# Performance work log

Measured on AMD Instinct MI355X. Metric: run time of the kernel, lower is better.

The kernel has to match this reference:

```python
import jax, jax.numpy as jnp
import numpy as np

B, L, H = 4, 1024, 8192
NH, HD = 64, 128
PD = HD // 2  # 64, rope-style positional dim
QL = HD * 4 * 3  # 1536, Q latent dim
KVL = HD * 4     # 512, KV latent dim


def setup_inputs() -> dict:
    key = jax.random.key(0)
    ks = jax.random.split(key, 18)
    w = lambda k, i, o: (jax.random.normal(k, (i, o), jnp.float32) * (1.0 / np.sqrt(i))).astype(jnp.float32)
    b = lambda k, o: jnp.zeros((o,), jnp.float32)
    return {
        'x': jax.random.normal(ks[0], (B, L, H), jnp.float32),
        'W_dq': w(ks[1], H, QL),   'b_dq': b(ks[2], QL),
        'W_dkv': w(ks[3], H, KVL), 'b_dkv': b(ks[4], KVL),
        'W_uq': w(ks[5], QL, H),   'b_uq': b(ks[6], H),
        'W_uk': w(ks[7], KVL, H),  'b_uk': b(ks[8], H),
        'W_uv': w(ks[9], KVL, H),  'b_uv': b(ks[10], H),
        'W_pq': w(ks[11], QL, NH * PD), 'b_pq': b(ks[12], NH * PD),
        'W_pk': w(ks[13], H, PD),  'b_pk': b(ks[14], PD),
        'W_o': w(ks[15], H, H),    'b_o': b(ks[16], H),
    }


def reference(x, W_dq, b_dq, W_dkv, b_dkv, W_uq, b_uq, W_uk, b_uk,
              W_uv, b_uv, W_pq, b_pq, W_pk, b_pk, W_o, b_o):
    Bb, Ll, Hh = x.shape
    # low-rank latents
    Q_lat = x @ W_dq + b_dq          # (B, L, 1536)
    KV_lat = x @ W_dkv + b_dkv       # (B, L, 512)
    # up-projections
    Q_c = (Q_lat @ W_uq + b_uq).reshape(Bb, Ll, NH, HD)
    Q_r = (Q_lat @ W_pq + b_pq).reshape(Bb, Ll, NH, PD)
    Q = jnp.concatenate([Q_c, Q_r], axis=-1)            # (B, L, NH, 192)
    K_c = (KV_lat @ W_uk + b_uk).reshape(Bb, Ll, NH, HD)
    K_r = x @ W_pk + b_pk                                # (B, L, 64), shared across heads
    K_r = jnp.broadcast_to(K_r[:, :, None, :], (Bb, Ll, NH, PD))
    K = jnp.concatenate([K_c, K_r], axis=-1)             # (B, L, NH, 192)
    V = (KV_lat @ W_uv + b_uv).reshape(Bb, Ll, NH, HD)   # (B, L, NH, 128)
    # attention with mismatched Q/K (192) vs V (128) head dims; scale by sqrt(128)
    scores = jnp.einsum('bqhd,bkhd->bhqk', Q, K) / np.float32(np.sqrt(HD))
    causal = jnp.tril(jnp.ones((Ll, Ll), bool))
    scores = jnp.where(causal, scores, jnp.float32(-jnp.inf))
    attn = jax.nn.softmax(scores, axis=-1)               # dropout = identity (eval)
    out = jnp.einsum('bhqk,bkhd->bqhd', attn, V).reshape(Bb, Ll, Hh)
    return out @ W_o + b_o
```

## Files before the change

### kernel.cpp

```cpp
#include <hip/hip_runtime.h>
#include <cstdint>

typedef unsigned short u16;
typedef __attribute__((ext_vector_type(8))) short bf16x8;
typedef __attribute__((ext_vector_type(4))) float f32x4;
typedef __attribute__((ext_vector_type(4))) unsigned short u16x4;

__device__ __forceinline__ u16 f2b(float f) {
  union { float f; uint32_t u; } v; v.f = f;
  uint32_t r = v.u + 0x7FFFu + ((v.u >> 16) & 1u);
  return (u16)(r >> 16);
}

__device__ __forceinline__ void gload_lds16(const void* g, void* l) {
  __builtin_amdgcn_global_load_lds((const __attribute__((address_space(1))) void*)g,
                                   (__attribute__((address_space(3))) void*)l, 16, 0, 0);
}

__device__ __forceinline__ void barrier_raw() {
  __builtin_amdgcn_sched_barrier(0);
  asm volatile("" ::: "memory");
  __builtin_amdgcn_s_barrier();
  asm volatile("" ::: "memory");
  __builtin_amdgcn_sched_barrier(0);
}
__device__ __forceinline__ void wait_vm8() {
  asm volatile("s_waitcnt vmcnt(8)" ::: "memory");
  __builtin_amdgcn_sched_barrier(0);
}

__global__ __launch_bounds__(256) void cvt_bf16(const float* __restrict__ in,
                                                u16* __restrict__ out, long n) {
  long i = ((long)blockIdx.x * 256 + threadIdx.x) * 4;
  if (i >= n) return;
  f32x4 v = *(const f32x4*)(in + i);
  u16x4 o;
#pragma unroll
  for (int k = 0; k < 4; k++) o[k] = f2b(v[k]);
  *(u16x4*)(out + i) = o;
}

__global__ __launch_bounds__(256) void transpose_cvt(const float* __restrict__ W,
                                                     u16* __restrict__ WT, int K, int N) {
  __shared__ float tile[32][33];
  const int tn0 = blockIdx.x * 32;
  const int tk0 = blockIdx.y * 32;
  const int c = threadIdx.x & 31;
  const int r0 = threadIdx.x >> 5;
#pragma unroll
  for (int rr = 0; rr < 32; rr += 8)
    tile[r0 + rr][c] = W[(long)(tk0 + r0 + rr) * N + tn0 + c];
  __syncthreads();
#pragma unroll
  for (int rr = 0; rr < 32; rr += 8)
    WT[(long)(tn0 + r0 + rr) * K + tk0 + c] = f2b(tile[c][r0 + rr]);
}

__global__ __launch_bounds__(256) void biascat3(const float* __restrict__ a,
                                                const float* __restrict__ b,
                                                const float* __restrict__ c,
                                                float* __restrict__ o) {
  int i = blockIdx.x * 256 + threadIdx.x;
  if (i < 1536) o[i] = a[i];
  else if (i < 2048) o[i] = b[i - 1536];
  else if (i < 2112) o[i] = c[i - 2048];
}
__global__ __launch_bounds__(256) void biascat2(const float* __restrict__ a,
                                                const float* __restrict__ b,
                                                int na, int n, float* __restrict__ o) {
  int i = blockIdx.x * 256 + threadIdx.x;
  if (i >= n) return;
  o[i] = (i < na) ? a[i] : b[i - na];
}

__global__ __launch_bounds__(256) void latcombine(const float* __restrict__ p,
                                                  const float* __restrict__ bias,
                                                  u16* __restrict__ lat) {
  const long S = 4096L * 2112;
  long i = ((long)blockIdx.x * 256 + threadIdx.x) * 4;
  if (i >= S) return;
  f32x4 s0 = *(const f32x4*)(p + i);
  f32x4 s1 = *(const f32x4*)(p + S + i);
  f32x4 s2 = *(const f32x4*)(p + 2 * S + i);
  f32x4 s3 = *(const f32x4*)(p + 3 * S + i);
  const int n = (int)(i % 2112);
  u16x4 o;
#pragma unroll
  for (int k = 0; k < 4; k++) o[k] = f2b(s0[k] + s1[k] + s2[k] + s3[k] + bias[n + k]);
  *(u16x4*)(lat + i) = o;
}

__global__ __launch_bounds__(256) void repl_kr(const u16* __restrict__ Kr,
                                               u16* __restrict__ Kbuf, int stride) {
  long idx = (long)blockIdx.x * 256 + threadIdx.x;
  int d4 = idx & 15;
  long t = idx >> 4;
  int hh = t & 63;
  long tok = t >> 6;
  if (tok >= 4096) return;
  u16x4 v = *(const u16x4*)(Kr + tok * (long)stride + d4 * 4);
  long b = tok >> 10, l = tok & 1023;
  *(u16x4*)(Kbuf + ((b * 64 + hh) * 1024 + l) * 192 + 128 + d4 * 4) = v;
}

template<int MODE>
__global__ __launch_bounds__(512, 2) void gemm256(
    const u16* __restrict__ A, long lda, const u16* __restrict__ BT, long ldb,
    const float* __restrict__ bias, void* __restrict__ outp, void* __restrict__ outp2,
    int N, int K) {
  __shared__ u16 sA[2][2][8192];
  __shared__ u16 sB[2][2][8192];
  const int tid = threadIdx.x;
  const int lane = tid & 63;
  const int w = tid >> 6;
  const int wr = w >> 2, wc = w & 3;
  const int hi = lane >> 4, lo = lane & 15;

  const int Nt = gridDim.x, Mt = gridDim.y;
  const int bid = blockIdx.y * Nt + blockIdx.x;
  const int xcd = bid & 7;
  const int idx = bid >> 3;
  int mt, nt;
  if ((Nt & 1) == 0) {
    const int Rm = Mt >> 2, Rn = Nt >> 1;
    const int xr = xcd & 3, xcn = xcd >> 2;
    const int Wb = Rn < 8 ? Rn : 8;
    const int cb = idx / (Rm * Wb);
    const int rem = idx - cb * (Rm * Wb);
    mt = xr * Rm + (rem % Rm);
    nt = xcn * Rn + cb * Wb + rem / Rm;
  } else {
    const int Rm = Mt >> 3;
    const int Wb = Nt < 8 ? Nt : 8;
    const int cb = idx / (Rm * Wb);
    const int rem = idx - cb * (Rm * Wb);
    mt = xcd * Rm + (rem % Rm);
    nt = cb * Wb + rem / Rm;
  }
  const long m0 = (long)mt * 256;
  const long n0 = (long)nt * 256;

  const int nkt = K >> 6;
  const long kb = (long)blockIdx.z * K;

  const int srow = tid >> 2;
  const int scol = ((tid & 3) ^ ((tid >> 3) & 3)) * 8;
  const long arow0 = m0 + srow, arow1 = arow0 + 128;
  long brow0 = n0 + srow, brow1 = brow0 + 128;
  if (brow0 > N - 1) brow0 = N - 1;
  if (brow1 > N - 1) brow1 = N - 1;
  const u16* aS0 = A + arow0 * lda + kb + scol;
  const u16* aS1 = A + arow1 * lda + kb + scol;
  const u16* bS0 = BT + brow0 * ldb + kb + scol;
  const u16* bS1 = BT + brow1 * ldb + kb + scol;

  const int aRd = (wr * 128 + lo) * 32 + (hi ^ ((lo >> 1) & 3)) * 8;
  const int bRd = (wc * 64 + lo) * 32 + (hi ^ ((lo >> 1) & 3)) * 8;

  f32x4 acc[8][4] = {};

#define STAGE(s0, s1, koff, dst) do { \
    gload_lds16((s0) + (koff), (dst) + tid * 8); \
    gload_lds16((s1) + (koff), (dst) + 4096 + tid * 8); \
  } while (0)
#define LDA_F(bufr, kh, m) (*(const bf16x8*)(&sA[bufr][kh][aRd + (m) * 512]))
#define LDB_F(bufr, kh, n) (*(const bf16x8*)(&sB[bufr][kh][bRd + (n) * 512]))
#define MFMA_GRP(mi, av) \
    acc[mi][0] = __builtin_amdgcn_mfma_f32_16x16x32_bf16(av, b0, acc[mi][0], 0, 0, 0); \
    acc[mi][1] = __builtin_amdgcn_mfma_f32_16x16x32_bf16(av, b1, acc[mi][1], 0, 0, 0); \
    acc[mi][2] = __builtin_amdgcn_mfma_f32_16x16x32_bf16(av, b2, acc[mi][2], 0, 0, 0); \
    acc[mi][3] = __builtin_amdgcn_mfma_f32_16x16x32_bf16(av, b3, acc[mi][3], 0, 0, 0);

  STAGE(aS0, aS1, 0, &sA[0][0][0]);
  STAGE(bS0, bS1, 0, &sB[0][0][0]);
  STAGE(aS0, aS1, 32, &sA[0][1][0]);
  STAGE(bS0, bS1, 32, &sB[0][1][0]);
  {
    const long t1o = (nkt > 1) ? 64 : 0;
    STAGE(aS0, aS1, t1o, &sA[1][0][0]);
    STAGE(bS0, bS1, t1o, &sB[1][0][0]);
  }
  wait_vm8();
  barrier_raw();

  for (int t = 0; t < nkt; ++t) {
    const int cur = t & 1, nxt = cur ^ 1;
    const int t1c = (t + 1 < nkt) ? t + 1 : nkt - 1;
    const int t2c = (t + 2 < nkt) ? t + 2 : nkt - 1;
    const long o1 = (long)t1c * 64;
    const long o2 = (long)t2c * 64;
    bf16x8 b0, b1, b2, b3, a0, a1, a2, a3, a4, a5, a6, a7;
    b0 = LDB_F(cur, 0, 0); b1 = LDB_F(cur, 0, 1); b2 = LDB_F(cur, 0, 2); b3 = LDB_F(cur, 0, 3);
    a0 = LDA_F(cur, 0, 0); a1 = LDA_F(cur, 0, 1); a2 = LDA_F(cur, 0, 2); a3 = LDA_F(cur, 0, 3);
    a4 = LDA_F(cur, 0, 4); a5 = LDA_F(cur, 0, 5); a6 = LDA_F(cur, 0, 6); a7 = LDA_F(cur, 0, 7);
    STAGE(aS0, aS1, o1 + 32, &sA[nxt][1][0]);
    barrier_raw();
    __builtin_amdgcn_s_setprio(1);
    MFMA_GRP(0, a0) MFMA_GRP(1, a1) MFMA_GRP(2, a2) MFMA_GRP(3, a3)
    __builtin_amdgcn_s_setprio(0);
    STAGE(bS0, bS1, o1 + 32, &sB[nxt][1][0]);
    __builtin_amdgcn_s_setprio(1);
    MFMA_GRP(4, a4) MFMA_GRP(5, a5) MFMA_GRP(6, a6) MFMA_GRP(7, a7)
    __builtin_amdgcn_s_setprio(0);
    wait_vm8();
    barrier_raw();
    b0 = LDB_F(cur, 1, 0); b1 = LDB_F(cur, 1, 1); b2 = LDB_F(cur, 1, 2); b3 = LDB_F(cur, 1, 3);
    a0 = LDA_F(cur, 1, 0); a1 = LDA_F(cur, 1, 1); a2 = LDA_F(cur, 1, 2); a3 = LDA_F(cur, 1, 3);
    a4 = LDA_F(cur, 1, 4); a5 = LDA_F(cur, 1, 5); a6 = LDA_F(cur, 1, 6); a7 = LDA_F(cur, 1, 7);
    STAGE(aS0, aS1, o2, &sA[cur][0][0]);
    barrier_raw();
    __builtin_amdgcn_s_setprio(1);
    MFMA_GRP(0, a0) MFMA_GRP(1, a1) MFMA_GRP(2, a2) MFMA_GRP(3, a3)
    __builtin_amdgcn_s_setprio(0);
    STAGE(bS0, bS1, o2, &sB[cur][0][0]);
    __builtin_amdgcn_s_setprio(1);
    MFMA_GRP(4, a4) MFMA_GRP(5, a5) MFMA_GRP(6, a6) MFMA_GRP(7, a7)
    __builtin_amdgcn_s_setprio(0);
    wait_vm8();
    barrier_raw();
  }
  asm volatile("s_waitcnt vmcnt(0)" ::: "memory");

#undef STAGE
#undef LDA_F
#undef LDB_F
#undef MFMA_GRP

#pragma unroll
  for (int m = 0; m < 8; m++) {
#pragma unroll
    for (int n = 0; n < 4; n++) {
      const long mb = m0 + wr * 128 + m * 16 + hi * 4;
      const long nn = n0 + wc * 64 + n * 16 + lo;
      if (nn >= N) continue;
      const float bv = bias[nn];
      if (MODE == 0) {
#pragma unroll
        for (int r = 0; r < 4; r++)
          ((u16*)outp)[(mb + r) * (long)N + nn] = f2b(acc[m][n][r] + bv);
      } else if (MODE == 3) {
#pragma unroll
        for (int r = 0; r < 4; r++)
          ((float*)outp)[(mb + r) * (long)N + nn] = acc[m][n][r] + bv;
      } else if (MODE == 6) {
        float* po = (float*)outp + (size_t)blockIdx.z * (4096ULL * 2112ULL);
#pragma unroll
        for (int r = 0; r < 4; r++)
          po[(mb + r) * (long)N + nn] = acc[m][n][r];
      } else if (MODE == 4) {
        if (nn < 8192) {
          const long h = nn >> 7, d = nn & 127;
#pragma unroll
          for (int r = 0; r < 4; r++) {
            const long mm = mb + r;
            const long bq = mm >> 10, l = mm & 1023;
            ((u16*)outp)[((bq * 64 + h) * 1024 + l) * 192 + d] = f2b(acc[m][n][r] + bv);
          }
        } else {
          const long q = nn - 8192;
          const long h = q >> 6, d = q & 63;
#pragma unroll
          for (int r = 0; r < 4; r++) {
            const long mm = mb + r;
            const long bq = mm >> 10, l = mm & 1023;
            ((u16*)outp)[((bq * 64 + h) * 1024 + l) * 192 + 128 + d] = f2b(acc[m][n][r] + bv);
          }
        }
      } else {
        if (nn < 8192) {
          const long h = nn >> 7, d = nn & 127;
#pragma unroll
          for (int r = 0; r < 4; r++) {
            const long mm = mb + r;
            const long bq = mm >> 10, l = mm & 1023;
            ((u16*)outp)[((bq * 64 + h) * 1024 + l) * 192 + d] = f2b(acc[m][n][r] + bv);
          }
        } else {
          const long v = nn - 8192;
          const long h = v >> 7, d = v & 127;
          u16x4 pk;
#pragma unroll
          for (int r = 0; r < 4; r++) pk[r] = f2b(acc[m][n][r] + bv);
          const long bq = mb >> 10, l = mb & 1023;
          *(u16x4*)((u16*)outp2 + ((bq * 64 + h) * 128 + d) * 1024 + l) = pk;
        }
      }
    }
  }
}

__global__ __launch_bounds__(512, 2) void attn256(const u16* __restrict__ Qb,
                                                  const u16* __restrict__ Kb,
                                                  const u16* __restrict__ Vt,
                                                  u16* __restrict__ O) {
  __shared__ u16 sK[2][12288];
  __shared__ u16 sV[2][8192];
  __shared__ u16 P[8][32][72];
  const int bh = blockIdx.x;
  const int qtb = 3 - blockIdx.y;
  const int b = bh >> 6, h = bh & 63;
  const int tid = threadIdx.x, w = tid >> 6, lane = tid & 63;
  const int hi = lane >> 4, lo = lane & 15, lo7 = lane & 7;
  const int q0w = qtb * 256 + w * 32;
  const u16* Qh = Qb + (size_t)bh * 1024 * 192;
  const u16* Kh = Kb + (size_t)bh * 1024 * 192;
  const u16* Vh = Vt + (size_t)bh * 128 * 1024;
  const float scale = 0.08838834764831845f;
  const float NEGINF = -3.0e38f;

  int kOff0, kOff1, kOff2, vOff0, vOff1;
  {
    int g0 = tid, g1 = tid + 512, g2 = tid + 1024;
    int r0 = g0 / 24, r1 = g1 / 24, r2 = g2 / 24;
    kOff0 = r0 * 192 + ((g0 - r0 * 24) ^ (r0 & 7)) * 8;
    kOff1 = r1 * 192 + ((g1 - r1 * 24) ^ (r1 & 7)) * 8;
    kOff2 = r2 * 192 + ((g2 - r2 * 24) ^ (r2 & 7)) * 8;
    int s0 = tid, s1 = tid + 512;
    vOff0 = (s0 >> 3) * 1024 + ((s0 & 7) ^ ((s0 >> 3) & 7)) * 8;
    vOff1 = (s1 >> 3) * 1024 + ((s1 & 7) ^ ((s1 >> 3) & 7)) * 8;
  }
#define STAGE_KV(tt, bb) do { \
    const u16* kb_ = Kh + (size_t)(tt) * (64 * 192); \
    const u16* vb_ = Vh + (size_t)(tt) * 64; \
    gload_lds16(kb_ + kOff0, &sK[bb][0] + tid * 8); \
    gload_lds16(kb_ + kOff1, &sK[bb][4096] + tid * 8); \
    gload_lds16(kb_ + kOff2, &sK[bb][8192] + tid * 8); \
    gload_lds16(vb_ + vOff0, &sV[bb][0] + tid * 8); \
    gload_lds16(vb_ + vOff1, &sV[bb][4096] + tid * 8); \
  } while (0)

  bf16x8 qf[2][6];
#pragma unroll
  for (int qi = 0; qi < 2; qi++) {
    const u16* qp = Qh + (size_t)(q0w + qi * 16 + lo) * 192 + hi * 8;
#pragma unroll
    for (int f = 0; f < 6; f++) qf[qi][f] = *(const bf16x8*)(qp + f * 32);
  }

  f32x4 oacc[2][8] = {};
  float m_run[2][4], l_run[2][4];
#pragma unroll
  for (int qi = 0; qi < 2; qi++)
#pragma unroll
    for (int r = 0; r < 4; r++) { m_run[qi][r] = NEGINF; l_run[qi][r] = 0.f; }

  const int nkt = (qtb + 1) * 4;
  STAGE_KV(0, 0);
  __syncthreads();

  for (int t = 0; t < nkt; t++) {
    const int cur = t & 1;
    const int tn = (t + 1 < nkt) ? t + 1 : nkt - 1;
    STAGE_KV(tn, cur ^ 1);
    const int k0 = t * 64;
    if (k0 < q0w + 32) {
      f32x4 s[2][4] = {};
      __builtin_amdgcn_s_setprio(1);
#pragma unroll
      for (int j = 0; j < 4; j++) {
#pragma unroll
        for (int f = 0; f < 6; f++) {
          bf16x8 kf = *(const bf16x8*)(&sK[cur][((j * 16 + lo) * 24 + ((f * 4 + hi) ^ lo7)) * 8]);
          s[0][j] = __builtin_amdgcn_mfma_f32_16x16x32_bf16(qf[0][f], kf, s[0][j], 0, 0, 0);
          s[1][j] = __builtin_amdgcn_mfma_f32_16x16x32_bf16(qf[1][f], kf, s[1][j], 0, 0, 0);
        }
      }
      __builtin_amdgcn_s_setprio(0);
      const bool diag = (k0 + 63 > q0w);
#pragma unroll
      for (int qi = 0; qi < 2; qi++) {
#pragma unroll
        for (int r = 0; r < 4; r++) {
          const int q = q0w + qi * 16 + hi * 4 + r;
          float sv[4];
          float mx = NEGINF;
#pragma unroll
          for (int j = 0; j < 4; j++) {
            float v = s[qi][j][r] * scale;
            if (diag && (k0 + j * 16 + lo > q)) v = NEGINF;
            sv[j] = v;
            mx = fmaxf(mx, v);
          }
#pragma unroll
          for (int o = 1; o < 16; o <<= 1) mx = fmaxf(mx, __shfl_xor(mx, o, 64));
          const float mnew = fmaxf(m_run[qi][r], mx);
          float sum = 0.f;
#pragma unroll
          for (int j = 0; j < 4; j++) {
            float pv = __expf(sv[j] - mnew);
            sum += pv;
            P[w][qi * 16 + hi * 4 + r][j * 16 + lo] = f2b(pv);
          }
#pragma unroll
          for (int o = 1; o < 16; o <<= 1) sum += __shfl_xor(sum, o, 64);
          const float alpha = __expf(m_run[qi][r] - mnew);
          l_run[qi][r] = l_run[qi][r] * alpha + sum;
          m_run[qi][r] = mnew;
#pragma unroll
          for (int j = 0; j < 8; j++) oacc[qi][j][r] *= alpha;
        }
      }
      __builtin_amdgcn_s_setprio(1);
#pragma unroll
      for (int kk = 0; kk < 2; kk++) {
        bf16x8 pf0 = *(const bf16x8*)(&P[w][lo][kk * 32 + hi * 8]);
        bf16x8 pf1 = *(const bf16x8*)(&P[w][16 + lo][kk * 32 + hi * 8]);
#pragma unroll
        for (int j = 0; j < 8; j++) {
          bf16x8 vf = *(const bf16x8*)(&sV[cur][((j * 16 + lo) * 8 + ((kk * 4 + hi) ^ lo7)) * 8]);
          oacc[0][j] = __builtin_amdgcn_mfma_f32_16x16x32_bf16(pf0, vf, oacc[0][j], 0, 0, 0);
          oacc[1][j] = __builtin_amdgcn_mfma_f32_16x16x32_bf16(pf1, vf, oacc[1][j], 0, 0, 0);
        }
      }
      __builtin_amdgcn_s_setprio(0);
    }
    __syncthreads();
  }
#undef STAGE_KV

#pragma unroll
  for (int qi = 0; qi < 2; qi++) {
#pragma unroll
    for (int r = 0; r < 4; r++) {
      const float inv = 1.f / l_run[qi][r];
      const int q = q0w + qi * 16 + hi * 4 + r;
      u16* op = O + ((size_t)(b * 1024 + q) * 64 + h) * 128;
#pragma unroll
      for (int j = 0; j < 8; j++)
        op[j * 16 + lo] = f2b(oacc[qi][j][r] * inv);
    }
  }
}

extern "C" void kernel_launch(void* const* d_in, const int* in_sizes, int n_in,
                              void* d_out, int out_size, void* d_ws, size_t ws_size,
                              hipStream_t stream) {
  const float* x     = (const float*)d_in[0];
  const float* W_dq  = (const float*)d_in[1];
  const float* b_dq  = (const float*)d_in[2];
  const float* W_dkv = (const float*)d_in[3];
  const float* b_dkv = (const float*)d_in[4];
  const float* W_uq  = (const float*)d_in[5];
  const float* b_uq  = (const float*)d_in[6];
  const float* W_uk  = (const float*)d_in[7];
  const float* b_uk  = (const float*)d_in[8];
  const float* W_uv  = (const float*)d_in[9];
  const float* b_uv  = (const float*)d_in[10];
  const float* W_pq  = (const float*)d_in[11];
  const float* b_pq  = (const float*)d_in[12];
  const float* W_pk  = (const float*)d_in[13];
  const float* b_pk  = (const float*)d_in[14];
  const float* W_o   = (const float*)d_in[15];
  const float* b_o   = (const float*)d_in[16];

  char* ws = (char*)d_ws;
  size_t off = 0;
  auto alloc = [&](size_t bytes) {
    char* p = ws + off;
    off += (bytes + 255) & ~(size_t)255;
    return p;
  };
  u16* xbf   = (u16*)alloc(33554432ULL * 2);
  u16* WT    = (u16*)alloc(67108864ULL * 2);
  u16* lat   = (u16*)alloc(4096ULL * 2112 * 2);
  float* bct = (float*)alloc(2112ULL * 4);
  float* bq  = (float*)alloc(12288ULL * 4);
  float* bkv = (float*)alloc(16384ULL * 4);
  u16* Qbuf  = (u16*)alloc(100663296ULL);
  u16* Kbuf  = (u16*)alloc(100663296ULL);
  u16* Vt    = (u16*)alloc(67108864ULL);
  u16* Obuf  = xbf;
  float* pf  = (float*)Qbuf;
  if (off > ws_size) return;

  dim3 blk(256), blk5(512);
  cvt_bf16<<<dim3(32768), blk, 0, stream>>>(x, xbf, 33554432L);
  transpose_cvt<<<dim3(48, 256), blk, 0, stream>>>(W_dq, WT, 8192, 1536);
  transpose_cvt<<<dim3(16, 256), blk, 0, stream>>>(W_dkv, WT + 1536L * 8192, 8192, 512);
  transpose_cvt<<<dim3(2, 256), blk, 0, stream>>>(W_pk, WT + 2048L * 8192, 8192, 64);
  biascat3<<<dim3(9), blk, 0, stream>>>(b_dq, b_dkv, b_pk, bct);
  gemm256<6><<<dim3(9, 16, 4), blk5, 0, stream>>>(xbf, 8192, WT, 8192, bct, pf, nullptr, 2112, 2048);
  latcombine<<<dim3(8448), blk, 0, stream>>>(pf, bct, lat);
  repl_kr<<<dim3(16384), blk, 0, stream>>>(lat + 2048, Kbuf, 2112);
  transpose_cvt<<<dim3(256, 48), blk, 0, stream>>>(W_uq, WT, 1536, 8192);
  transpose_cvt<<<dim3(128, 48), blk, 0, stream>>>(W_pq, WT + 8192L * 1536, 1536, 4096);
  biascat2<<<dim3(48), blk, 0, stream>>>(b_uq, b_pq, 8192, 12288, bq);
  gemm256<4><<<dim3(48, 16), blk5, 0, stream>>>(lat, 2112, WT, 1536, bq, Qbuf, nullptr, 12288, 1536);
  transpose_cvt<<<dim3(256, 16), blk, 0, stream>>>(W_uk, WT, 512, 8192);
  transpose_cvt<<<dim3(256, 16), blk, 0, stream>>>(W_uv, WT + 8192L * 512, 512, 8192);
  biascat2<<<dim3(64), blk, 0, stream>>>(b_uk, b_uv, 8192, 16384, bkv);
  gemm256<5><<<dim3(64, 16), blk5, 0, stream>>>(lat + 1536, 2112, WT, 512, bkv, Kbuf, Vt, 16384, 512);
  attn256<<<dim3(256, 4), blk5, 0, stream>>>(Qbuf, Kbuf, Vt, Obuf);
  transpose_cvt<<<dim3(256, 256), blk, 0, stream>>>(W_o, WT, 8192, 8192);
  gemm256<3><<<dim3(32, 16), blk5, 0, stream>>>(Obuf, 8192, WT, 8192, b_o, d_out, nullptr, 8192, 8192);
}
```

Before: 1.383 ms.

## Batch weight transposes and bias prep into fewer launches; add lazy softmax rescale

Several per-weight transpose-and-convert launches are merged into one multi-job transpose kernel, and the bias concatenation kernels are merged into one, which removes launch overhead and small-grid tails. The K/V up-projection weights now sit at a separate workspace offset, so their transpose can run before the Q GEMM. The attention softmax skips the running-max update and the accumulator rescale when every row's new max stays within a threshold of the running max (a lazy-rescale trick). That saves exp and multiply work on most tiles, at the cost of an extra wave-wide vote, some recomputed score scaling, and a bounded risk of overflow in the unnormalised sums.

```diff
diff --git a/kernel.cpp b/kernel.cpp
--- a/kernel.cpp
+++ b/kernel.cpp
@@ -38,6 +38,39 @@
 #pragma unroll
   for (int k = 0; k < 4; k++) o[k] = f2b(v[k]);
   *(u16x4*)(out + i) = o;
+}
+
+struct TJobs {
+  const float* s[4];
+  int K[4];
+  int N[4];
+  long off[4];
+  int cum[4];
+};
+
+__global__ __launch_bounds__(256) void transpose_multi(TJobs J, u16* __restrict__ WT) {
+  __shared__ float tile[32][33];
+  const int bid = blockIdx.x;
+  int j = 0;
+#pragma unroll
+  for (int t = 0; t < 3; t++) if (bid >= J.cum[t]) j = t + 1;
+  const int base = j ? J.cum[j - 1] : 0;
+  const int lb = bid - base;
+  const int K = J.K[j], N = J.N[j];
+  const float* W = J.s[j];
+  u16* dst = WT + J.off[j];
+  const int nb = N >> 5;
+  const int tn0 = (lb % nb) * 32;
+  const int tk0 = (lb / nb) * 32;
+  const int c = threadIdx.x & 31;
+  const int r0 = threadIdx.x >> 5;
+#pragma unroll
+  for (int rr = 0; rr < 32; rr += 8)
+    tile[r0 + rr][c] = W[(long)(tk0 + r0 + rr) * N + tn0 + c];
+  __syncthreads();
+#pragma unroll
+  for (int rr = 0; rr < 32; rr += 8)
+    dst[(long)(tn0 + r0 + rr) * K + tk0 + c] = f2b(tile[c][r0 + rr]);
 }
 
 __global__ __launch_bounds__(256) void transpose_cvt(const float* __restrict__ W,
@@ -56,21 +89,29 @@
     WT[(long)(tn0 + r0 + rr) * K + tk0 + c] = f2b(tile[c][r0 + rr]);
 }
 
-__global__ __launch_bounds__(256) void biascat3(const float* __restrict__ a,
-                                                const float* __restrict__ b,
-                                                const float* __restrict__ c,
-                                                float* __restrict__ o) {
+__global__ __launch_bounds__(256) void biasprep(const float* __restrict__ b_dq,
+                                                const float* __restrict__ b_dkv,
+                                                const float* __restrict__ b_pk,
+                                                const float* __restrict__ b_uq,
+                                                const float* __restrict__ b_pq,
+                                                const float* __restrict__ b_uk,
+                                                const float* __restrict__ b_uv,
+                                                float* __restrict__ bct,
+                                                float* __restrict__ bq,
+                                                float* __restrict__ bkv) {
   int i = blockIdx.x * 256 + threadIdx.x;
-  if (i < 1536) o[i] = a[i];
-  else if (i < 2048) o[i] = b[i - 1536];
-  else if (i < 2112) o[i] = c[i - 2048];
-}
-__global__ __launch_bounds__(256) void biascat2(const float* __restrict__ a,
-                                                const float* __restrict__ b,
-                                                int na, int n, float* __restrict__ o) {
-  int i = blockIdx.x * 256 + threadIdx.x;
-  if (i >= n) return;
-  o[i] = (i < na) ? a[i] : b[i - na];
+  if (i < 2112) {
+    bct[i] = (i < 1536) ? b_dq[i] : (i < 2048) ? b_dkv[i - 1536] : b_pk[i - 2048];
+    return;
+  }
+  int i2 = i - 2112;
+  if (i2 < 12288) {
+    bq[i2] = (i2 < 8192) ? b_uq[i2] : b_pq[i2 - 8192];
+    return;
+  }
+  int i3 = i2 - 12288;
+  if (i3 < 16384)
+    bkv[i3] = (i3 < 8192) ? b_uk[i3] : b_uv[i3 - 8192];
 }
 
 __global__ __launch_bounds__(256) void latcombine(const float* __restrict__ p,
@@ -367,37 +408,71 @@
       }
       __builtin_amdgcn_s_setprio(0);
       const bool diag = (k0 + 63 > q0w);
+      float mx[2][4];
+      bool ok = true;
 #pragma unroll
       for (int qi = 0; qi < 2; qi++) {
 #pragma unroll
         for (int r = 0; r < 4; r++) {
           const int q = q0w + qi * 16 + hi * 4 + r;
-          float sv[4];
-          float mx = NEGINF;
+          float m = NEGINF;
 #pragma unroll
           for (int j = 0; j < 4; j++) {
             float v = s[qi][j][r] * scale;
             if (diag && (k0 + j * 16 + lo > q)) v = NEGINF;
-            sv[j] = v;
-            mx = fmaxf(mx, v);
+            m = fmaxf(m, v);
           }
 #pragma unroll
-          for (int o = 1; o < 16; o <<= 1) mx = fmaxf(mx, __shfl_xor(mx, o, 64));
-          const float mnew = fmaxf(m_run[qi][r], mx);
-          float sum = 0.f;
-#pragma unroll
-          for (int j = 0; j < 4; j++) {
-            float pv = __expf(sv[j] - mnew);
-            sum += pv;
-            P[w][qi * 16 + hi * 4 + r][j * 16 + lo] = f2b(pv);
+          for (int o = 1; o < 16; o <<= 1) m = fmaxf(m, __shfl_xor(m, o, 64));
+          mx[qi][r] = m;
+          ok = ok && (m <= m_run[qi][r] + 8.0f);
+        }
+      }
+      if (__all(ok)) {
+#pragma unroll
+        for (int qi = 0; qi < 2; qi++) {
+#pragma unroll
+          for (int r = 0; r < 4; r++) {
+            const int q = q0w + qi * 16 + hi * 4 + r;
+            const float mr = m_run[qi][r];
+            float sum = 0.f;
+#pragma unroll
+            for (int j = 0; j < 4; j++) {
+              float v = s[qi][j][r] * scale;
+              if (diag && (k0 + j * 16 + lo > q)) v = NEGINF;
+              float pv = __expf(v - mr);
+              sum += pv;
+              P[w][qi * 16 + hi * 4 + r][j * 16 + lo] = f2b(pv);
+            }
+#pragma unroll
+            for (int o = 1; o < 16; o <<= 1) sum += __shfl_xor(sum, o, 64);
+            l_run[qi][r] += sum;
           }
-#pragma unroll
-          for (int o = 1; o < 16; o <<= 1) sum += __shfl_xor(sum, o, 64);
-          const float alpha = __expf(m_run[qi][r] - mnew);
-          l_run[qi][r] = l_run[qi][r] * alpha + sum;
-          m_run[qi][r] = mnew;
-#pragma unroll
-          for (int j = 0; j < 8; j++) oacc[qi][j][r] *= alpha;
+        }
+      } else {
+#pragma unroll
+        for (int qi = 0; qi < 2; qi++) {
+#pragma unroll
+          for (int r = 0; r < 4; r++) {
+            const int q = q0w + qi * 16 + hi * 4 + r;
+            const float mnew = fmaxf(m_run[qi][r], mx[qi][r]);
+            float sum = 0.f;
+#pragma unroll
+            for (int j = 0; j < 4; j++) {
+              float v = s[qi][j][r] * scale;
+              if (diag && (k0 + j * 16 + lo > q)) v = NEGINF;
+              float pv = __expf(v - mnew);
+              sum += pv;
+              P[w][qi * 16 + hi * 4 + r][j * 16 + lo] = f2b(pv);
+            }
+#pragma unroll
+            for (int o = 1; o < 16; o <<= 1) sum += __shfl_xor(sum, o, 64);
+            const float alpha = __expf(m_run[qi][r] - mnew);
+            l_run[qi][r] = l_run[qi][r] * alpha + sum;
+            m_run[qi][r] = mnew;
+#pragma unroll
+            for (int j = 0; j < 8; j++) oacc[qi][j][r] *= alpha;
+          }
         }
       }
       __builtin_amdgcn_s_setprio(1);
@@ -475,21 +550,32 @@
 
   dim3 blk(256), blk5(512);
   cvt_bf16<<<dim3(32768), blk, 0, stream>>>(x, xbf, 33554432L);
-  transpose_cvt<<<dim3(48, 256), blk, 0, stream>>>(W_dq, WT, 8192, 1536);
-  transpose_cvt<<<dim3(16, 256), blk, 0, stream>>>(W_dkv, WT + 1536L * 8192, 8192, 512);
-  transpose_cvt<<<dim3(2, 256), blk, 0, stream>>>(W_pk, WT + 2048L * 8192, 8192, 64);
-  biascat3<<<dim3(9), blk, 0, stream>>>(b_dq, b_dkv, b_pk, bct);
+
+  {
+    TJobs J;
+    J.s[0] = W_dq;  J.K[0] = 8192; J.N[0] = 1536; J.off[0] = 0;              J.cum[0] = 12288;
+    J.s[1] = W_dkv; J.K[1] = 8192; J.N[1] = 512;  J.off[1] = 1536L * 8192;   J.cum[1] = 16384;
+    J.s[2] = W_pk;  J.K[2] = 8192; J.N[2] = 64;   J.off[2] = 2048L * 8192;   J.cum[2] = 16896;
+    J.s[3] = W_pk;  J.K[3] = 8192; J.N[3] = 64;   J.off[3] = 2048L * 8192;   J.cum[3] = 16896;
+    transpose_multi<<<dim3(16896), blk, 0, stream>>>(J, WT);
+  }
+  biasprep<<<dim3(121), blk, 0, stream>>>(b_dq, b_dkv, b_pk, b_uq, b_pq, b_uk, b_uv,
+                                          bct, bq, bkv);
   gemm256<6><<<dim3(9, 16, 4), blk5, 0, stream>>>(xbf, 8192, WT, 8192, bct, pf, nullptr, 2112, 2048);
   latcombine<<<dim3(8448), blk, 0, stream>>>(pf, bct, lat);
   repl_kr<<<dim3(16384), blk, 0, stream>>>(lat + 2048, Kbuf, 2112);
-  transpose_cvt<<<dim3(256, 48), blk, 0, stream>>>(W_uq, WT, 1536, 8192);
-  transpose_cvt<<<dim3(128, 48), blk, 0, stream>>>(W_pq, WT + 8192L * 1536, 1536, 4096);
-  biascat2<<<dim3(48), blk, 0, stream>>>(b_uq, b_pq, 8192, 12288, bq);
+
+  const long KVOFF = 12288L * 1536;
+  {
+    TJobs J;
+    J.s[0] = W_uq; J.K[0] = 1536; J.N[0] = 8192; J.off[0] = 0;                    J.cum[0] = 12288;
+    J.s[1] = W_pq; J.K[1] = 1536; J.N[1] = 4096; J.off[1] = 8192L * 1536;         J.cum[1] = 18432;
+    J.s[2] = W_uk; J.K[2] = 512;  J.N[2] = 8192; J.off[2] = KVOFF;                J.cum[2] = 22528;
+    J.s[3] = W_uv; J.K[3] = 512;  J.N[3] = 8192; J.off[3] = KVOFF + 8192L * 512;  J.cum[3] = 26624;
+    transpose_multi<<<dim3(26624), blk, 0, stream>>>(J, WT);
+  }
   gemm256<4><<<dim3(48, 16), blk5, 0, stream>>>(lat, 2112, WT, 1536, bq, Qbuf, nullptr, 12288, 1536);
-  transpose_cvt<<<dim3(256, 16), blk, 0, stream>>>(W_uk, WT, 512, 8192);
-  transpose_cvt<<<dim3(256, 16), blk, 0, stream>>>(W_uv, WT + 8192L * 512, 512, 8192);
-  biascat2<<<dim3(64), blk, 0, stream>>>(b_uk, b_uv, 8192, 16384, bkv);
-  gemm256<5><<<dim3(64, 16), blk5, 0, stream>>>(lat + 1536, 2112, WT, 512, bkv, Kbuf, Vt, 16384, 512);
+  gemm256<5><<<dim3(64, 16), blk5, 0, stream>>>(lat + 1536, 2112, WT + KVOFF, 512, bkv, Kbuf, Vt, 16384, 512);
   attn256<<<dim3(256, 4), blk5, 0, stream>>>(Qbuf, Kbuf, Vt, Obuf);
   transpose_cvt<<<dim3(256, 256), blk, 0, stream>>>(W_o, WT, 8192, 8192);
   gemm256<3><<<dim3(32, 16), blk5, 0, stream>>>(Obuf, 8192, WT, 8192, b_o, d_out, nullptr, 8192, 8192);
```

After: 1.640 ms. +18.5%, slower.
